# Optimization experiments

Hardware: AMD Instinct MI355X
Metric: run time of the kernel (lower is better)

## Reference

```python
import jax, jax.numpy as jnp
import numpy as np

NQ = 8          # n_qubits
NC = 4          # n_cycles of the angle encoder
PI = np.float32(np.pi)
LAYER_QUBITS = [[0, 1, 2, 3, 4, 5, 6, 7], [1, 3, 5, 7]]  # active qubits per conv layer
FINAL_QUBITS = [3, 7]                                    # active after last pooling
CX = jnp.array([[1, 0, 0, 0], [0, 1, 0, 0], [0, 0, 0, 1], [0, 0, 1, 0]], jnp.complex64)


def apply1(psi, U, q):
    """Apply 1-qubit gate U ((2,2) shared or (B,2,2) batched) on qubit q. psi: (B,2,...,2)."""
    psi = jnp.moveaxis(psi, 1 + q, -1)
    if U.ndim == 3:
        psi = jnp.einsum('bij,b...j->b...i', U, psi)
    else:
        psi = jnp.einsum('ij,...j->...i', U, psi)
    return jnp.moveaxis(psi, -1, 1 + q)


def apply2(psi, U, q0, q1):
    """Apply 2-qubit gate U (4,4) on (q0,q1); q0 is the more-significant wire."""
    psi = jnp.moveaxis(psi, (1 + q0, 1 + q1), (-2, -1))
    sh = psi.shape
    psi = jnp.einsum('ij,...j->...i', U, psi.reshape(sh[:-2] + (4,)))
    return jnp.moveaxis(psi.reshape(sh), (-2, -1), (1 + q0, 1 + q1))


def rz_mat(t):
    return jnp.array([[jnp.exp(-0.5j * t), 0.0], [0.0, jnp.exp(0.5j * t)]]).astype(jnp.complex64)


def ry_mat(t):
    c, s = jnp.cos(t / 2), jnp.sin(t / 2)
    return jnp.array([[c, -s], [s, c]]).astype(jnp.complex64)


def crx_mat(t):
    c = jnp.cos(t / 2).astype(jnp.complex64)
    s = jnp.sin(t / 2).astype(jnp.complex64)
    M = jnp.eye(4, dtype=jnp.complex64)
    return M.at[2, 2].set(c).at[3, 3].set(c).at[2, 3].set(-1j * s).at[3, 2].set(-1j * s)


def u3_mat(t, p, l):
    c, s = jnp.cos(t / 2), jnp.sin(t / 2)
    return jnp.array([[c + 0j, -jnp.exp(1j * l) * s],
                      [jnp.exp(1j * p) * s, jnp.exp(1j * (p + l)) * c]]).astype(jnp.complex64)


def expz(psi, q):
    """<Z_q> = P(q=0) - P(q=1)."""
    p = psi.real ** 2 + psi.imag ** 2
    p = jnp.moveaxis(p, 1 + q, 1).reshape(p.shape[0], 2, -1).sum(-1)
    return p[:, 0] - p[:, 1]


def encode(x):
    """Angle-encoding circuit (circuit_builder): NC cycles of RY(x) + CNOT ring."""
    B = x.shape[0]
    psi = jnp.zeros((B, 2 ** NQ), jnp.complex64).at[:, 0].set(1.0).reshape((B,) + (2,) * NQ)
    for c in range(NC):
        ang = x[:, c * NQ:(c + 1) * NQ]
        cc, ss = jnp.cos(ang / 2), jnp.sin(ang / 2)
        for q in range(NQ):
            U = jnp.stack([jnp.stack([cc[:, q], -ss[:, q]], -1),
                           jnp.stack([ss[:, q], cc[:, q]], -1)], -2).astype(jnp.complex64)
            psi = apply1(psi, U, q)
        for q in range(NQ):
            psi = apply2(psi, CX, q, (q + 1) % NQ)
    return psi


def forward(x, rz_p, ry_p, ry2_p, crx_p, u3_p, u3b_p, W1, b1, W2, b2):
    psi0 = encode(x)
    psi1 = psi0  # deepcopy of encoded state for the second feature map
    for layer in range(2):
        aq = LAYER_QUBITS[layer]
        n = len(aq)
        RZp, RYp, RY2p = rz_mat(rz_p[layer]), ry_mat(ry_p[layer]), ry_mat(ry2_p[layer])
        RZm, RZpl = rz_mat(-PI / 2), rz_mat(PI / 2)
        # circuit 1: ZNOTY-style conv blocks, even pairs then odd pairs
        for parity in (0, 1):
            for i in range(parity, n - 1, 2):
                qc, qt = aq[i], aq[i + 1]
                psi0 = apply1(psi0, RZm, qt)
                psi0 = apply2(psi0, CX, qt, qc)
                psi0 = apply1(psi0, RZp, qc)
                psi0 = apply1(psi0, RYp, qt)
                psi0 = apply2(psi0, CX, qc, qt)
                psi0 = apply1(psi0, RY2p, qt)
                psi0 = apply2(psi0, CX, qt, qc)
                psi0 = apply1(psi0, RZpl, qc)
        remain = [aq[i] for i in range(n) if i % 2 == 1]
        U3a = u3_mat(u3_p[layer, 0], u3_p[layer, 1], u3_p[layer, 2])
        for q in remain:
            psi0 = apply1(psi0, U3a, q)
        # circuit 2: CRX conv blocks, even pairs then odd pairs
        CRXp = crx_mat(crx_p[layer])
        for parity in (0, 1):
            for i in range(parity, n - 1, 2):
                psi1 = apply2(psi1, CRXp, aq[i], aq[i + 1])
        U3b = u3_mat(u3b_p[layer, 0], u3b_p[layer, 1], u3b_p[layer, 2])
        for q in remain:
            psi1 = apply1(psi1, U3b, q)
    xv = jnp.stack([expz(psi0, q) for q in FINAL_QUBITS], 1)  # (B,2)
    yv = jnp.stack([expz(psi1, q) for q in FINAL_QUBITS], 1)  # (B,2)
    feat = jnp.concatenate([xv, yv], 1)                       # (B,4)
    h = jnp.tanh(feat @ W1.T + b1)
    return jax.nn.sigmoid(h @ W2.T + b2)


def setup_inputs() -> dict:
    key = jax.random.key(0)
    ks = jax.random.split(key, 12)
    B = 8192
    return {
        'x': jax.random.normal(ks[0], (B, NC * NQ), jnp.float32),
        'rz_p': jax.random.normal(ks[1], (2,), jnp.float32) * 0.5,
        'ry_p': jax.random.normal(ks[2], (2,), jnp.float32) * 0.5,
        'ry2_p': jax.random.normal(ks[3], (2,), jnp.float32) * 0.5,
        'crx_p': jax.random.normal(ks[4], (2,), jnp.float32) * 0.5,
        'u3_p': jax.random.normal(ks[5], (2, 3), jnp.float32) * 0.5,
        'u3b_p': jax.random.normal(ks[6], (2, 3), jnp.float32) * 0.5,
        'W1': jax.random.normal(ks[7], (15, 4), jnp.float32) * 0.4,
        'b1': jax.random.normal(ks[8], (15,), jnp.float32) * 0.1,
        'W2': jax.random.normal(ks[9], (1, 15), jnp.float32) * 0.25,
        'b2': jax.random.normal(ks[10], (1,), jnp.float32) * 0.1,
    }


def reference(x, rz_p, ry_p, ry2_p, crx_p, u3_p, u3b_p, W1, b1, W2, b2):
    return forward(x, rz_p, ry_p, ry2_p, crx_p, u3_p, u3b_p, W1, b1, W2, b2)
```

## Files before the change

kernel.cpp:

```cpp
#include <hip/hip_runtime.h>

#define DEV __device__ __forceinline__


DEV int lpar(int lane, int m) { return __builtin_popcount(lane & m) & 1; }
constexpr int cpar(int v) { return (v ^ (v >> 1) ^ (v >> 2) ^ (v >> 3)) & 1; }

constexpr int TLm(int LM, int SM) { return (LM << 2) | (SM >> 2); }
constexpr int TSm(int SM) { return SM & 3; }

template<int LM, int SM, int LR, int SR>
DEV void ryr(float* p, float gc, float gs, int lane) {
  const float sg0 = lpar(lane, LR) ? gs : -gs;
  const float sg1 = -sg0;
  if constexpr (LM != 0) {
    float t[4];
    #pragma unroll
    for (int s = 0; s < 4; ++s) t[s] = __shfl_xor(p[s ^ SM], LM);
    #pragma unroll
    for (int s = 0; s < 4; ++s)
      p[s] = gc * p[s] + (cpar(s & SR) ? sg1 : sg0) * t[s];
  } else {
    constexpr int LOW = SM & (-SM);
    #pragma unroll
    for (int s = 0; s < 4; ++s) if (!(s & LOW)) {
      const int s1 = s ^ SM;
      float a = p[s], b = p[s1];
      float sg = cpar(s & SR) ? sg1 : sg0;
      p[s]  = gc * a + sg * b;
      p[s1] = gc * b - sg * a;
    }
  }
}

template<int LM, int SM, int LR, int SR>
DEV void u3_g(float* pr, float* pi, const float* u, int lane) {
  const bool hl = lpar(lane, LR);
  const float d0r = hl ? u[6] : u[0], d0i = hl ? u[7] : u[1];
  const float o0r = hl ? u[4] : u[2], o0i = hl ? u[5] : u[3];
  const float d1r = hl ? u[0] : u[6], d1i = hl ? u[1] : u[7];
  const float o1r = hl ? u[2] : u[4], o1i = hl ? u[3] : u[5];
  if constexpr (LM != 0) {
    float tr[4], ti[4];
    #pragma unroll
    for (int s = 0; s < 4; ++s) {
      tr[s] = __shfl_xor(pr[s ^ SM], LM);
      ti[s] = __shfl_xor(pi[s ^ SM], LM);
    }
    #pragma unroll
    for (int s = 0; s < 4; ++s) {
      const bool c1 = cpar(s & SR);
      const float dr = c1 ? d1r : d0r, di = c1 ? d1i : d0i;
      const float orr = c1 ? o1r : o0r, oi = c1 ? o1i : o0i;
      float ar = pr[s], ai = pi[s];
      pr[s] = dr*ar - di*ai + orr*tr[s] - oi*ti[s];
      pi[s] = dr*ai + di*ar + orr*ti[s] + oi*tr[s];
    }
  } else {
    constexpr int LOW = SM & (-SM);
    #pragma unroll
    for (int s = 0; s < 4; ++s) if (!(s & LOW)) {
      const int s1 = s ^ SM;
      const bool c1 = cpar(s & SR);
      const float dAr = c1 ? d1r : d0r, dAi = c1 ? d1i : d0i;
      const float oAr = c1 ? o1r : o0r, oAi = c1 ? o1i : o0i;
      const float dBr = c1 ? d0r : d1r, dBi = c1 ? d0i : d1i;
      const float oBr = c1 ? o0r : o1r, oBi = c1 ? o0i : o1i;
      float ar = pr[s], ai = pi[s], br = pr[s1], bi = pi[s1];
      pr[s]  = dAr*ar - dAi*ai + oAr*br - oAi*bi;
      pi[s]  = dAr*ai + dAi*ar + oAr*bi + oAi*br;
      pr[s1] = dBr*br - dBi*bi + oBr*ar - oBi*ai;
      pi[s1] = dBr*bi + dBi*br + oBr*ai + oBi*ar;
    }
  }
}

template<int LMt, int SMt, int LRc, int SRc>
DEV void crx_g(float* pr, float* pi, float c, float s_, int lane) {
  const bool hl = lpar(lane, LRc);
  const float cc0 = hl ? c : 1.0f, ss0 = hl ? s_ : 0.0f;
  const float cc1 = hl ? 1.0f : c, ss1 = hl ? 0.0f : s_;
  if constexpr (LMt != 0) {
    float tr[4], ti[4];
    #pragma unroll
    for (int s = 0; s < 4; ++s) {
      tr[s] = __shfl_xor(pr[s ^ SMt], LMt);
      ti[s] = __shfl_xor(pi[s ^ SMt], LMt);
    }
    #pragma unroll
    for (int s = 0; s < 4; ++s) {
      const bool c1 = cpar(s & SRc);
      const float cc = c1 ? cc1 : cc0, ss = c1 ? ss1 : ss0;
      float ar = pr[s], ai = pi[s];
      pr[s] = cc * ar + ss * ti[s];
      pi[s] = cc * ai - ss * tr[s];
    }
  } else {
    constexpr int LOW = SMt & (-SMt);
    #pragma unroll
    for (int s = 0; s < 4; ++s) if (!(s & LOW)) {
      const int s1 = s ^ SMt;
      const bool c1 = cpar(s & SRc);
      const float cc = c1 ? cc1 : cc0, ss = c1 ? ss1 : ss0;
      float ar = pr[s], ai = pi[s], br = pr[s1], bi = pi[s1];
      pr[s]  = cc * ar + ss * bi;
      pi[s]  = cc * ai - ss * br;
      pr[s1] = cc * br + ss * ai;
      pi[s1] = cc * bi - ss * ar;
    }
  }
}

#define U4CLASS(Q)                                                            \
  if constexpr (!(((SRc == 0) && (Q & 2)) || ((SRt == 0) && (Q & 1)))) {      \
    const int r1 = R ^ Q, r2 = r1 ^ 2;                                        \
    const float2 wd = w2[r1 * 4 + r1],       wo = w2[r1 * 4 + (r1 ^ 1)];      \
    const float2 vd = w2[r2 * 4 + r1],       vo = w2[r2 * 4 + (r1 ^ 1)];      \
    _Pragma("unroll")                                                         \
    for (int s = 0; s < 4; ++s)                                               \
      if (((cpar(s & SRc) << 1) | cpar(s & SRt)) == Q) {                      \
        float ar = pr[s], ai = pi[s], br = tr[s], bi = ti[s];                 \
        pr[s] = wd.x*ar - wd.y*ai + wo.x*br - wo.y*bi;                        \
        pi[s] = wd.x*ai + wd.y*ar + wo.x*bi + wo.y*br;                        \
        tr[s] = vd.x*ar - vd.y*ai + vo.x*br - vo.y*bi;                        \
        ti[s] = vd.x*ai + vd.y*ar + vo.x*bi + vo.y*br;                        \
      }                                                                       \
  }

template<int LMc, int SMc, int LMt, int SMt, int LRc, int SRc, int LRt, int SRt>
DEV void u4_g(float* pr, float* pi, const float2* w2, int lane) {
  const int R = (lpar(lane, LRc) << 1) | lpar(lane, LRt);
  float tr[4], ti[4];
  #pragma unroll
  for (int s = 0; s < 4; ++s) {
    float vr = pr[s ^ SMt], vi = pi[s ^ SMt];
    if constexpr (LMt != 0) { vr = __shfl_xor(vr, LMt); vi = __shfl_xor(vi, LMt); }
    tr[s] = vr; ti[s] = vi;
  }
  U4CLASS(0) U4CLASS(1) U4CLASS(2) U4CLASS(3)
  #pragma unroll
  for (int s = 0; s < 4; ++s) {
    float br = tr[s ^ SMc], bi = ti[s ^ SMc];
    if constexpr (LMc != 0) { br = __shfl_xor(br, LMc); bi = __shfl_xor(bi, LMc); }
    pr[s] += br; pi[s] += bi;
  }
}

template<int LMc,int SMc,int LMt,int SMt,int LRc,int SRc,int LRt,int SRt>
DEV void u4o(float* pr, float* pi, const float2* w2, int lane) {
  u4_g<TLm(LMc,SMc),TSm(SMc), TLm(LMt,SMt),TSm(SMt),
       TLm(LRc,SRc),TSm(SRc), TLm(LRt,SRt),TSm(SRt)>(pr, pi, w2, lane);
}
template<int LM,int SM,int LR,int SR>
DEV void u3o(float* pr, float* pi, const float* u, int lane) {
  u3_g<TLm(LM,SM),TSm(SM), TLm(LR,SR),TSm(SR)>(pr, pi, u, lane);
}
template<int LMt,int SMt,int LRc,int SRc>
DEV void crxo(float* pr, float* pi, float c, float s_, int lane) {
  crx_g<TLm(LMt,SMt),TSm(SMt), TLm(LRc,SRc),TSm(SRc)>(pr, pi, c, s_, lane);
}

DEV void u3_make(float t, float p, float l, float* u) {
  float c = __cosf(0.5f * t), s = __sinf(0.5f * t);
  float cp = __cosf(p), sp = __sinf(p);
  float cl = __cosf(l), sl = __sinf(l);
  float cpl = __cosf(p + l), spl = __sinf(p + l);
  u[0] = c;        u[1] = 0.0f;
  u[2] = -cl * s;  u[3] = -sl * s;
  u[4] = cp * s;   u[5] = sp * s;
  u[6] = cpl * c;  u[7] = spl * c;
}

DEV void expz_fin(const float* pr, const float* pi, int lane, float& z3, float& z7) {
  float t3 = 0.0f, t7 = 0.0f;
  #pragma unroll
  for (int s = 0; s < 4; ++s) {
    float p = pr[s] * pr[s] + pi[s] * pi[s];
    t7 += p;
    t3 += (s & 1) ? -p : p;
  }
  if (lpar(lane, 40)) { t3 = -t3; t7 = -t7; }
  #pragma unroll
  for (int m = 1; m < 64; m <<= 1) {
    t3 += __shfl_xor(t3, m);
    t7 += __shfl_xor(t7, m);
  }
  z3 = t3; z7 = t7;
}


__global__ __launch_bounds__(1024, 4)
void qcnn_kernel(const float* __restrict__ x,
                 const float* __restrict__ rz_p, const float* __restrict__ ry_p,
                 const float* __restrict__ ry2_p, const float* __restrict__ crx_p,
                 const float* __restrict__ u3_p, const float* __restrict__ u3b_p,
                 const float* __restrict__ W1, const float* __restrict__ b1,
                 const float* __restrict__ W2, const float* __restrict__ b2,
                 float* __restrict__ out, int B) {
  __shared__ __align__(8) float cw[64];

  const int tid  = threadIdx.x;
  const int lane = tid & 63;
  const int wave = tid >> 6;
  const int sub  = lane & 15;
  const int elem  = blockIdx.x * 16 + wave;
  const int elemc = elem < B ? elem : (B - 1);

  if (tid < 32) {
    const int lay = tid >> 4, e = tid & 15, i4 = e >> 2, j4 = e & 3;
    const int base = tid & 48;
    const float c45 = 0.70710678118654752f;
    float rz = rz_p[lay], ry = ry_p[lay], ry2 = ry2_p[lay];
    float mr = (i4 == j4) ? c45 : 0.0f;
    float mi = (i4 == j4) ? ((i4 & 1) ? -c45 : c45) : 0.0f;
    { int t = (i4 & 1) ? (i4 ^ 2) : i4; int src = base | (t << 2) | j4;
      mr = __shfl(mr, src); mi = __shfl(mi, src); }
    { float cz = __cosf(0.5f * rz), sz = __sinf(0.5f * rz);
      float di = (i4 & 2) ? sz : -sz;
      float nr = cz * mr - di * mi, ni = cz * mi + di * mr; mr = nr; mi = ni; }
    { float cy = __cosf(0.5f * ry), sy = __sinf(0.5f * ry);
      int src = base | ((i4 ^ 1) << 2) | j4;
      float orr = __shfl(mr, src), oii = __shfl(mi, src);
      float sg = (i4 & 1) ? sy : -sy;
      mr = cy * mr + sg * orr; mi = cy * mi + sg * oii; }
    { int t = (i4 & 2) ? (i4 ^ 1) : i4; int src = base | (t << 2) | j4;
      mr = __shfl(mr, src); mi = __shfl(mi, src); }
    { float cy = __cosf(0.5f * ry2), sy = __sinf(0.5f * ry2);
      int src = base | ((i4 ^ 1) << 2) | j4;
      float orr = __shfl(mr, src), oii = __shfl(mi, src);
      float sg = (i4 & 1) ? sy : -sy;
      mr = cy * mr + sg * orr; mi = cy * mi + sg * oii; }
    { int t = (i4 & 1) ? (i4 ^ 2) : i4; int src = base | (t << 2) | j4;
      mr = __shfl(mr, src); mi = __shfl(mi, src); }
    { float di = (i4 & 2) ? c45 : -c45;
      float nr = c45 * mr - di * mi, ni = c45 * mi + di * mr; mr = nr; mi = ni; }
    cw[(lay * 16 + e) * 2]     = mr;
    cw[(lay * 16 + e) * 2 + 1] = mi;
  }

  float2 aa = ((const float2*)x)[(size_t)elemc * 16 + sub];
  float ch0 = __cosf(0.5f * aa.x), sh0 = __sinf(0.5f * aa.x);
  float ch1 = __cosf(0.5f * aa.y), sh1 = __sinf(0.5f * aa.y);

  float cq[8], sq[8];
  #pragma unroll
  for (int q = 0; q < 8; ++q) {
    cq[q] = __shfl((q & 1) ? ch1 : ch0, q >> 1);
    sq[q] = __shfl((q & 1) ? sh1 : sh0, q >> 1);
  }

  float p[4];
  {
    float g = ((lane & 32) ? sq[0] : cq[0]) * ((lane & 16) ? sq[2] : cq[2]) *
              ((lane & 8)  ? sq[4] : cq[4]) * ((lane & 4)  ? sq[6] : cq[6]) *
              ((lane & 2)  ? sq[1] : cq[1]) * ((lane & 1)  ? sq[3] : cq[3]);
    p[0] = g * cq[5] * cq[7];
    p[1] = g * cq[5] * sq[7];
    p[2] = g * sq[5] * cq[7];
    p[3] = g * sq[5] * sq[7];
  }

  #define ENC(k, LM, SM, LR, SR) {                                  \
    float gc = __shfl(((k) & 1) ? ch1 : ch0, (k) >> 1);             \
    float gs = __shfl(((k) & 1) ? sh1 : sh0, (k) >> 1);             \
    ryr<TLm(LM,SM), TSm(SM), TLm(LR,SR), TSm(SR)>(p, gc, gs, lane); }

  ENC(8,  8,8, 7,15)  ENC(9,  4,8, 8,8)   ENC(10, 4,4, 12,8)  ENC(11, 2,4, 12,12)
  ENC(12, 2,2, 14,12) ENC(13, 1,2, 14,14) ENC(14, 1,1, 15,14) ENC(15, 8,9, 15,15)
  ENC(16, 12,0, 8,15) ENC(17, 0,12, 15,7) ENC(18, 6,0, 3,15)  ENC(19, 0,6, 15,3)
  ENC(20, 3,0, 1,15)  ENC(21, 0,3, 15,1)  ENC(22, 9,8, 0,15)  ENC(23, 4,9, 15,0)
  ENC(24, 12,12, 2,10) ENC(25, 6,12, 7,8) ENC(26, 6,6, 4,7)   ENC(27, 3,6, 11,4)
  ENC(28, 3,3, 10,11)  ENC(29, 9,11, 5,10) ENC(30, 13,1, 5,5) ENC(31, 8,5, 10,5)
  #undef ENC

  const float e0 = p[0], e1 = p[1], e2_ = p[2], e3 = p[3];

  __syncthreads();
  const float2* w0 = (const float2*)cw;
  const float2* w1 = ((const float2*)cw) + 16;

  float pi_[4] = {0.0f, 0.0f, 0.0f, 0.0f};

  u4o<10,0,  0,10, 8,10, 5,2 >(p, pi_, w0, lane);
  u4o<5,0,   0,5,  1,5,  10,1>(p, pi_, w0, lane);
  u4o<10,8,  4,10, 0,10, 5,0 >(p, pi_, w0, lane);
  u4o<5,4,   2,5,  0,5,  10,0>(p, pi_, w0, lane);
  u4o<0,10,  5,0,  5,2,  1,5 >(p, pi_, w0, lane);
  u4o<0,5,   10,8, 10,1, 0,10>(p, pi_, w0, lane);
  u4o<4,10,  5,4,  5,0,  0,5 >(p, pi_, w0, lane);
  {
    float ua[8]; u3_make(u3_p[0], u3_p[1], u3_p[2], ua);
    u3o<0,10, 5,2 >(p, pi_, ua, lane);
    u3o<0,5,  10,1>(p, pi_, ua, lane);
    u3o<4,10, 5,0 >(p, pi_, ua, lane);
    u3o<2,5,  10,0>(p, pi_, ua, lane);
  }
  u4o<0,10,  0,5,  5,2,  10,1>(p, pi_, w1, lane);
  u4o<4,10,  2,5,  5,0,  10,0>(p, pi_, w1, lane);
  u4o<0,5,   4,10, 10,1, 5,0 >(p, pi_, w1, lane);
  {
    float ua[8]; u3_make(u3_p[3], u3_p[4], u3_p[5], ua);
    u3o<0,5,  10,1>(p, pi_, ua, lane);
    u3o<2,5,  10,0>(p, pi_, ua, lane);
  }

  float f0, f1;
  expz_fin(p, pi_, lane, f0, f1);

  p[0] = e0; p[1] = e1; p[2] = e2_; p[3] = e3;
  pi_[0] = 0.0f; pi_[1] = 0.0f; pi_[2] = 0.0f; pi_[3] = 0.0f;

  {
    float t = crx_p[0];
    float cc = __cosf(0.5f * t), ss = __sinf(0.5f * t);
    crxo<0,10, 8,10>(p, pi_, cc, ss, lane);
    crxo<0,5,  1,5 >(p, pi_, cc, ss, lane);
    crxo<4,10, 0,10>(p, pi_, cc, ss, lane);
    crxo<2,5,  0,5 >(p, pi_, cc, ss, lane);
    crxo<5,0,  5,2 >(p, pi_, cc, ss, lane);
    crxo<10,8, 10,1>(p, pi_, cc, ss, lane);
    crxo<5,4,  5,0 >(p, pi_, cc, ss, lane);
  }
  {
    float ub[8]; u3_make(u3b_p[0], u3b_p[1], u3b_p[2], ub);
    u3o<0,10, 5,2 >(p, pi_, ub, lane);
    u3o<0,5,  10,1>(p, pi_, ub, lane);
    u3o<4,10, 5,0 >(p, pi_, ub, lane);
    u3o<2,5,  10,0>(p, pi_, ub, lane);
  }
  {
    float t = crx_p[1];
    float cc = __cosf(0.5f * t), ss = __sinf(0.5f * t);
    crxo<0,5,  5,2 >(p, pi_, cc, ss, lane);
    crxo<2,5,  5,0 >(p, pi_, cc, ss, lane);
    crxo<4,10, 10,1>(p, pi_, cc, ss, lane);
  }
  {
    float ub[8]; u3_make(u3b_p[3], u3b_p[4], u3b_p[5], ub);
    u3o<0,5,  10,1>(p, pi_, ub, lane);
    u3o<2,5,  10,0>(p, pi_, ub, lane);
  }

  float f2, f3;
  expz_fin(p, pi_, lane, f2, f3);

  const int j = (lane < 15) ? lane : 0;
  float acc = W1[j * 4 + 0] * f0 + W1[j * 4 + 1] * f1 +
              W1[j * 4 + 2] * f2 + W1[j * 4 + 3] * f3 + b1[j];
  float e2 = __expf(2.0f * acc);
  float th = (e2 - 1.0f) / (e2 + 1.0f);
  float part = (lane < 15) ? th * W2[j] : 0.0f;
  #pragma unroll
  for (int m = 1; m < 64; m <<= 1) part += __shfl_xor(part, m);

  if (lane == 0 && elem < B) {
    float z = part + b2[0];
    out[elem] = 1.0f / (1.0f + __expf(-z));
  }
}

extern "C" void kernel_launch(void* const* d_in, const int* in_sizes, int n_in,
                              void* d_out, int out_size, void* d_ws, size_t ws_size,
                              hipStream_t stream) {
  (void)n_in; (void)out_size; (void)d_ws; (void)ws_size;
  const float* x     = (const float*)d_in[0];
  const float* rz_p  = (const float*)d_in[1];
  const float* ry_p  = (const float*)d_in[2];
  const float* ry2_p = (const float*)d_in[3];
  const float* crx_p = (const float*)d_in[4];
  const float* u3_p  = (const float*)d_in[5];
  const float* u3b_p = (const float*)d_in[6];
  const float* W1    = (const float*)d_in[7];
  const float* b1    = (const float*)d_in[8];
  const float* W2    = (const float*)d_in[9];
  const float* b2    = (const float*)d_in[10];
  float* out = (float*)d_out;

  const int B = in_sizes[0] / 32;
  const int blocks = (B + 15) / 16;
  qcnn_kernel<<<dim3(blocks), dim3(1024), 0, stream>>>(
      x, rz_p, ry_p, ry2_p, crx_p, u3_p, u3b_p, W1, b1, W2, b2, out, B);
}
```

Before: 125.6 us.

## Map two batch elements per wavefront with 8 amplitudes per lane

Changes the state-vector distribution from 64 lanes holding 4 amplitudes each to 32 lanes holding 8 amplitudes, so each wave simulates two circuits at once. More qubits become in-register rather than cross-lane, which is meant to reduce shuffle traffic per amplitude. Reductions shorten to 32 lanes, and blocks shrink to 512 threads still covering 16 elements. In exchange it doubles register state per lane, which may lower occupancy, and the bit remapping of lane and register indices must stay consistent.

New measurement: 119.5 us. -4.9%, faster.

```diff
diff --git a/kernel.cpp b/kernel.cpp
--- a/kernel.cpp
+++ b/kernel.cpp
@@ -6,24 +6,24 @@
 DEV int lpar(int lane, int m) { return __builtin_popcount(lane & m) & 1; }
 constexpr int cpar(int v) { return (v ^ (v >> 1) ^ (v >> 2) ^ (v >> 3)) & 1; }
 
-constexpr int TLm(int LM, int SM) { return (LM << 2) | (SM >> 2); }
-constexpr int TSm(int SM) { return SM & 3; }
+constexpr int TLm(int LM, int SM) { return (LM << 1) | (SM >> 3); }
+constexpr int TSm(int SM) { return SM & 7; }
 
 template<int LM, int SM, int LR, int SR>
 DEV void ryr(float* p, float gc, float gs, int lane) {
   const float sg0 = lpar(lane, LR) ? gs : -gs;
   const float sg1 = -sg0;
   if constexpr (LM != 0) {
-    float t[4];
-    #pragma unroll
-    for (int s = 0; s < 4; ++s) t[s] = __shfl_xor(p[s ^ SM], LM);
-    #pragma unroll
-    for (int s = 0; s < 4; ++s)
+    float t[8];
+    #pragma unroll
+    for (int s = 0; s < 8; ++s) t[s] = __shfl_xor(p[s ^ SM], LM);
+    #pragma unroll
+    for (int s = 0; s < 8; ++s)
       p[s] = gc * p[s] + (cpar(s & SR) ? sg1 : sg0) * t[s];
   } else {
     constexpr int LOW = SM & (-SM);
     #pragma unroll
-    for (int s = 0; s < 4; ++s) if (!(s & LOW)) {
+    for (int s = 0; s < 8; ++s) if (!(s & LOW)) {
       const int s1 = s ^ SM;
       float a = p[s], b = p[s1];
       float sg = cpar(s & SR) ? sg1 : sg0;
@@ -41,14 +41,14 @@
   const float d1r = hl ? u[0] : u[6], d1i = hl ? u[1] : u[7];
   const float o1r = hl ? u[2] : u[4], o1i = hl ? u[3] : u[5];
   if constexpr (LM != 0) {
-    float tr[4], ti[4];
-    #pragma unroll
-    for (int s = 0; s < 4; ++s) {
+    float tr[8], ti[8];
+    #pragma unroll
+    for (int s = 0; s < 8; ++s) {
       tr[s] = __shfl_xor(pr[s ^ SM], LM);
       ti[s] = __shfl_xor(pi[s ^ SM], LM);
     }
     #pragma unroll
-    for (int s = 0; s < 4; ++s) {
+    for (int s = 0; s < 8; ++s) {
       const bool c1 = cpar(s & SR);
       const float dr = c1 ? d1r : d0r, di = c1 ? d1i : d0i;
       const float orr = c1 ? o1r : o0r, oi = c1 ? o1i : o0i;
@@ -59,7 +59,7 @@
   } else {
     constexpr int LOW = SM & (-SM);
     #pragma unroll
-    for (int s = 0; s < 4; ++s) if (!(s & LOW)) {
+    for (int s = 0; s < 8; ++s) if (!(s & LOW)) {
       const int s1 = s ^ SM;
       const bool c1 = cpar(s & SR);
       const float dAr = c1 ? d1r : d0r, dAi = c1 ? d1i : d0i;
@@ -81,14 +81,14 @@
   const float cc0 = hl ? c : 1.0f, ss0 = hl ? s_ : 0.0f;
   const float cc1 = hl ? 1.0f : c, ss1 = hl ? 0.0f : s_;
   if constexpr (LMt != 0) {
-    float tr[4], ti[4];
-    #pragma unroll
-    for (int s = 0; s < 4; ++s) {
+    float tr[8], ti[8];
+    #pragma unroll
+    for (int s = 0; s < 8; ++s) {
       tr[s] = __shfl_xor(pr[s ^ SMt], LMt);
       ti[s] = __shfl_xor(pi[s ^ SMt], LMt);
     }
     #pragma unroll
-    for (int s = 0; s < 4; ++s) {
+    for (int s = 0; s < 8; ++s) {
       const bool c1 = cpar(s & SRc);
       const float cc = c1 ? cc1 : cc0, ss = c1 ? ss1 : ss0;
       float ar = pr[s], ai = pi[s];
@@ -98,7 +98,7 @@
   } else {
     constexpr int LOW = SMt & (-SMt);
     #pragma unroll
-    for (int s = 0; s < 4; ++s) if (!(s & LOW)) {
+    for (int s = 0; s < 8; ++s) if (!(s & LOW)) {
       const int s1 = s ^ SMt;
       const bool c1 = cpar(s & SRc);
       const float cc = c1 ? cc1 : cc0, ss = c1 ? ss1 : ss0;
@@ -117,7 +117,7 @@
     const float2 wd = w2[r1 * 4 + r1],       wo = w2[r1 * 4 + (r1 ^ 1)];      \
     const float2 vd = w2[r2 * 4 + r1],       vo = w2[r2 * 4 + (r1 ^ 1)];      \
     _Pragma("unroll")                                                         \
-    for (int s = 0; s < 4; ++s)                                               \
+    for (int s = 0; s < 8; ++s)                                               \
       if (((cpar(s & SRc) << 1) | cpar(s & SRt)) == Q) {                      \
         float ar = pr[s], ai = pi[s], br = tr[s], bi = ti[s];                 \
         pr[s] = wd.x*ar - wd.y*ai + wo.x*br - wo.y*bi;                        \
@@ -130,16 +130,16 @@
 template<int LMc, int SMc, int LMt, int SMt, int LRc, int SRc, int LRt, int SRt>
 DEV void u4_g(float* pr, float* pi, const float2* w2, int lane) {
   const int R = (lpar(lane, LRc) << 1) | lpar(lane, LRt);
-  float tr[4], ti[4];
-  #pragma unroll
-  for (int s = 0; s < 4; ++s) {
+  float tr[8], ti[8];
+  #pragma unroll
+  for (int s = 0; s < 8; ++s) {
     float vr = pr[s ^ SMt], vi = pi[s ^ SMt];
     if constexpr (LMt != 0) { vr = __shfl_xor(vr, LMt); vi = __shfl_xor(vi, LMt); }
     tr[s] = vr; ti[s] = vi;
   }
   U4CLASS(0) U4CLASS(1) U4CLASS(2) U4CLASS(3)
   #pragma unroll
-  for (int s = 0; s < 4; ++s) {
+  for (int s = 0; s < 8; ++s) {
     float br = tr[s ^ SMc], bi = ti[s ^ SMc];
     if constexpr (LMc != 0) { br = __shfl_xor(br, LMc); bi = __shfl_xor(bi, LMc); }
     pr[s] += br; pi[s] += bi;
@@ -174,14 +174,14 @@
 DEV void expz_fin(const float* pr, const float* pi, int lane, float& z3, float& z7) {
   float t3 = 0.0f, t7 = 0.0f;
   #pragma unroll
-  for (int s = 0; s < 4; ++s) {
+  for (int s = 0; s < 8; ++s) {
     float p = pr[s] * pr[s] + pi[s] * pi[s];
     t7 += p;
     t3 += (s & 1) ? -p : p;
   }
-  if (lpar(lane, 40)) { t3 = -t3; t7 = -t7; }
-  #pragma unroll
-  for (int m = 1; m < 64; m <<= 1) {
+  if (lpar(lane, 20)) { t3 = -t3; t7 = -t7; }
+  #pragma unroll
+  for (int m = 1; m < 32; m <<= 1) {
     t3 += __shfl_xor(t3, m);
     t7 += __shfl_xor(t7, m);
   }
@@ -189,7 +189,7 @@
 }
 
 
-__global__ __launch_bounds__(1024, 4)
+__global__ __launch_bounds__(512, 2)
 void qcnn_kernel(const float* __restrict__ x,
                  const float* __restrict__ rz_p, const float* __restrict__ ry_p,
                  const float* __restrict__ ry2_p, const float* __restrict__ crx_p,
@@ -203,7 +203,10 @@
   const int lane = tid & 63;
   const int wave = tid >> 6;
   const int sub  = lane & 15;
-  const int elem  = blockIdx.x * 16 + wave;
+  const int half = lane >> 5;
+  const int l5   = lane & 31;
+  const int hb   = lane & 32;
+  const int elem  = blockIdx.x * 16 + wave * 2 + half;
   const int elemc = elem < B ? elem : (B - 1);
 
   if (tid < 32) {
@@ -245,24 +248,24 @@
   float cq[8], sq[8];
   #pragma unroll
   for (int q = 0; q < 8; ++q) {
-    cq[q] = __shfl((q & 1) ? ch1 : ch0, q >> 1);
-    sq[q] = __shfl((q & 1) ? sh1 : sh0, q >> 1);
-  }
-
-  float p[4];
-  {
-    float g = ((lane & 32) ? sq[0] : cq[0]) * ((lane & 16) ? sq[2] : cq[2]) *
-              ((lane & 8)  ? sq[4] : cq[4]) * ((lane & 4)  ? sq[6] : cq[6]) *
-              ((lane & 2)  ? sq[1] : cq[1]) * ((lane & 1)  ? sq[3] : cq[3]);
-    p[0] = g * cq[5] * cq[7];
-    p[1] = g * cq[5] * sq[7];
-    p[2] = g * sq[5] * cq[7];
-    p[3] = g * sq[5] * sq[7];
+    cq[q] = __shfl((q & 1) ? ch1 : ch0, hb | (q >> 1));
+    sq[q] = __shfl((q & 1) ? sh1 : sh0, hb | (q >> 1));
+  }
+
+  float p[8];
+  {
+    float g = ((l5 & 16) ? sq[0] : cq[0]) * ((l5 & 8) ? sq[2] : cq[2]) *
+              ((l5 & 4)  ? sq[4] : cq[4]) * ((l5 & 2) ? sq[6] : cq[6]) *
+              ((l5 & 1)  ? sq[1] : cq[1]);
+    #pragma unroll
+    for (int s = 0; s < 8; ++s)
+      p[s] = g * ((s & 4) ? sq[3] : cq[3]) * ((s & 2) ? sq[5] : cq[5]) *
+                 ((s & 1) ? sq[7] : cq[7]);
   }
 
   #define ENC(k, LM, SM, LR, SR) {                                  \
-    float gc = __shfl(((k) & 1) ? ch1 : ch0, (k) >> 1);             \
-    float gs = __shfl(((k) & 1) ? sh1 : sh0, (k) >> 1);             \
+    float gc = __shfl(((k) & 1) ? ch1 : ch0, hb | ((k) >> 1));      \
+    float gs = __shfl(((k) & 1) ? sh1 : sh0, hb | ((k) >> 1));      \
     ryr<TLm(LM,SM), TSm(SM), TLm(LR,SR), TSm(SR)>(p, gc, gs, lane); }
 
   ENC(8,  8,8, 7,15)  ENC(9,  4,8, 8,8)   ENC(10, 4,4, 12,8)  ENC(11, 2,4, 12,12)
@@ -273,13 +276,17 @@
   ENC(28, 3,3, 10,11)  ENC(29, 9,11, 5,10) ENC(30, 13,1, 5,5) ENC(31, 8,5, 10,5)
   #undef ENC
 
-  const float e0 = p[0], e1 = p[1], e2_ = p[2], e3 = p[3];
+  float e_[8];
+  #pragma unroll
+  for (int s = 0; s < 8; ++s) e_[s] = p[s];
 
   __syncthreads();
   const float2* w0 = (const float2*)cw;
   const float2* w1 = ((const float2*)cw) + 16;
 
-  float pi_[4] = {0.0f, 0.0f, 0.0f, 0.0f};
+  float pi_[8];
+  #pragma unroll
+  for (int s = 0; s < 8; ++s) pi_[s] = 0.0f;
 
   u4o<10,0,  0,10, 8,10, 5,2 >(p, pi_, w0, lane);
   u4o<5,0,   0,5,  1,5,  10,1>(p, pi_, w0, lane);
@@ -307,8 +314,8 @@
   float f0, f1;
   expz_fin(p, pi_, lane, f0, f1);
 
-  p[0] = e0; p[1] = e1; p[2] = e2_; p[3] = e3;
-  pi_[0] = 0.0f; pi_[1] = 0.0f; pi_[2] = 0.0f; pi_[3] = 0.0f;
+  #pragma unroll
+  for (int s = 0; s < 8; ++s) { p[s] = e_[s]; pi_[s] = 0.0f; }
 
   {
     float t = crx_p[0];
@@ -344,16 +351,16 @@
   float f2, f3;
   expz_fin(p, pi_, lane, f2, f3);
 
-  const int j = (lane < 15) ? lane : 0;
+  const int j = (l5 < 15) ? l5 : 0;
   float acc = W1[j * 4 + 0] * f0 + W1[j * 4 + 1] * f1 +
               W1[j * 4 + 2] * f2 + W1[j * 4 + 3] * f3 + b1[j];
   float e2 = __expf(2.0f * acc);
   float th = (e2 - 1.0f) / (e2 + 1.0f);
-  float part = (lane < 15) ? th * W2[j] : 0.0f;
-  #pragma unroll
-  for (int m = 1; m < 64; m <<= 1) part += __shfl_xor(part, m);
-
-  if (lane == 0 && elem < B) {
+  float part = (l5 < 15) ? th * W2[j] : 0.0f;
+  #pragma unroll
+  for (int m = 1; m < 32; m <<= 1) part += __shfl_xor(part, m);
+
+  if (l5 == 0 && elem < B) {
     float z = part + b2[0];
     out[elem] = 1.0f / (1.0f + __expf(-z));
   }
@@ -378,6 +385,6 @@
 
   const int B = in_sizes[0] / 32;
   const int blocks = (B + 15) / 16;
-  qcnn_kernel<<<dim3(blocks), dim3(1024), 0, stream>>>(
+  qcnn_kernel<<<dim3(blocks), dim3(512), 0, stream>>>(
       x, rz_p, ry_p, ry2_p, crx_p, u3_p, u3b_p, W1, b1, W2, b2, out, B);
 }
```
